# Kernel optimization log

Measured on AMD Instinct MI355X. Metric: run time of the kernel, lower is better.

Reference implementation:

```python
import jax, jax.numpy as jnp
import numpy as np

B, S, T = 16, 128, 128
V_SRC = V_TGT = 32000
E = H = 512
NL = 4


def setup_inputs() -> dict:
    key = jax.random.key(0)
    ks = jax.random.split(key, 16)
    sc = 0.05
    return {
        "src": jax.random.randint(ks[0], (B, S), 0, V_SRC),
        "tgt": jax.random.randint(ks[1], (B, T), 0, V_TGT),
        "src_emb": jax.random.normal(ks[2], (V_SRC, E), jnp.float32) * sc,
        "tgt_emb": jax.random.normal(ks[3], (V_TGT, E), jnp.float32) * sc,
        # stacked per-layer LSTM params (E == H so all layers share shape)
        "enc_Wih": jax.random.normal(ks[4], (NL, 4 * H, E), jnp.float32) * sc,
        "enc_Whh": jax.random.normal(ks[5], (NL, 4 * H, H), jnp.float32) * sc,
        "enc_b": jax.random.normal(ks[6], (NL, 4 * H), jnp.float32) * sc,
        "dec_Wih": jax.random.normal(ks[7], (NL, 4 * H, E), jnp.float32) * sc,
        "dec_Whh": jax.random.normal(ks[8], (NL, 4 * H, H), jnp.float32) * sc,
        "dec_b": jax.random.normal(ks[9], (NL, 4 * H), jnp.float32) * sc,
        "fc_W": jax.random.normal(ks[10], (V_TGT, H), jnp.float32) * sc,
        "fc_b": jax.random.normal(ks[11], (V_TGT,), jnp.float32) * sc,
    }


def _lstm_layer(x, Wih, Whh, b, h0, c0):
    # x: [B,T,E]; PyTorch gate order i,f,g,o. Input GEMM hoisted out of scan.
    xW = jnp.einsum("bte,ge->btg", x, Wih) + b  # [B,T,4H]

    def step(carry, xw):
        h, c = carry
        g = xw + h @ Whh.T
        i, f, gg, o = jnp.split(g, 4, axis=-1)
        c = jax.nn.sigmoid(f) * c + jax.nn.sigmoid(i) * jnp.tanh(gg)
        h = jax.nn.sigmoid(o) * jnp.tanh(c)
        return (h, c), h

    (hT, cT), hs = jax.lax.scan(step, (h0, c0), jnp.swapaxes(xW, 0, 1))
    return jnp.swapaxes(hs, 0, 1), hT, cT


def _lstm_stack(x, Wih, Whh, b, h0s, c0s):
    hTs, cTs = [], []
    for l in range(NL):
        x, hT, cT = _lstm_layer(x, Wih[l], Whh[l], b[l], h0s[l], c0s[l])
        hTs.append(hT)
        cTs.append(cT)
    return x, jnp.stack(hTs), jnp.stack(cTs)


def reference(src, tgt, src_emb, tgt_emb, enc_Wih, enc_Whh, enc_b,
              dec_Wih, dec_Whh, dec_b, fc_W, fc_b):
    zeros = jnp.zeros((NL, B, H), jnp.float32)
    # encoder
    _, hN, cN = _lstm_stack(src_emb[src], enc_Wih, enc_Whh, enc_b, zeros, zeros)
    # decoder initialized from encoder final state (train branch)
    dec_out, _, _ = _lstm_stack(tgt_emb[tgt], dec_Wih, dec_Whh, dec_b, hN, cN)
    # vocab projection
    return dec_out @ fc_W.T + fc_b  # [B,T,V_TGT]
```

## Files before the change

kernel.cpp:

```cpp
#include <hip/hip_runtime.h>
#include <hip/hip_bf16.h>
#include <cstddef>

#define NL   4
#define BB   16
#define TT   128
#define HH   512
#define G4   2048
#define BT   2048
#define VV   32000

__global__ __launch_bounds__(128) void embed_kern(const int* __restrict__ idx,
                                                  const float* __restrict__ emb,
                                                  float* __restrict__ out) {
  int tk = blockIdx.x;
  int row = idx[tk];
  const float4* s = (const float4*)(emb + (size_t)row * HH);
  float4* d = (float4*)(out + (size_t)tk * HH);
  d[threadIdx.x] = s[threadIdx.x];
}

__global__ __launch_bounds__(256) void zero_kern(float* __restrict__ p, int n) {
  int i = blockIdx.x * 256 + threadIdx.x;
  if (i < n) p[i] = 0.f;
}
__global__ __launch_bounds__(256) void copy_kern(float* __restrict__ d,
                                                 const float* __restrict__ s, int n) {
  int i = blockIdx.x * 256 + threadIdx.x;
  if (i < n) d[i] = s[i];
}

#define BM 128
#define BN 64
#define BK 16
__global__ __launch_bounds__(256) void gemm_bias_kern(
    const float* __restrict__ A, const float* __restrict__ B,
    const float* __restrict__ bias, float* __restrict__ C,
    int M, int N, int K)
{
  __shared__ float As[BK][BM];
  __shared__ float Bs[BK][BN];
  const int tid = threadIdx.x;
  const int m0 = blockIdx.y * BM;
  const int n0 = blockIdx.x * BN;
  const int ty = tid >> 4;
  const int tx = tid & 15;

  float acc[8][4];
#pragma unroll
  for (int i = 0; i < 8; ++i)
#pragma unroll
    for (int j = 0; j < 4; ++j) acc[i][j] = 0.f;

  for (int k0 = 0; k0 < K; k0 += BK) {
#pragma unroll
    for (int i = 0; i < 2; ++i) {
      int f = tid * 2 + i;
      int row = f >> 2;
      int k4 = (f & 3) * 4;
      float4 v = *(const float4*)(A + (size_t)(m0 + row) * K + k0 + k4);
      As[k4 + 0][row] = v.x;
      As[k4 + 1][row] = v.y;
      As[k4 + 2][row] = v.z;
      As[k4 + 3][row] = v.w;
    }
    {
      int row = tid >> 2;
      int k4 = (tid & 3) * 4;
      float4 v = *(const float4*)(B + (size_t)(n0 + row) * K + k0 + k4);
      Bs[k4 + 0][row] = v.x;
      Bs[k4 + 1][row] = v.y;
      Bs[k4 + 2][row] = v.z;
      Bs[k4 + 3][row] = v.w;
    }
    __syncthreads();
#pragma unroll
    for (int k = 0; k < BK; ++k) {
      float4 a0 = *(const float4*)&As[k][ty * 8];
      float4 a1 = *(const float4*)&As[k][ty * 8 + 4];
      float4 bv = *(const float4*)&Bs[k][tx * 4];
      float av[8] = {a0.x, a0.y, a0.z, a0.w, a1.x, a1.y, a1.z, a1.w};
      float bb[4] = {bv.x, bv.y, bv.z, bv.w};
#pragma unroll
      for (int i = 0; i < 8; ++i)
#pragma unroll
        for (int j = 0; j < 4; ++j) acc[i][j] += av[i] * bb[j];
    }
    __syncthreads();
  }
#pragma unroll
  for (int i = 0; i < 8; ++i) {
    size_t row = (size_t)(m0 + ty * 8 + i);
#pragma unroll
    for (int j = 0; j < 4; ++j) {
      int col = n0 + tx * 4 + j;
      C[row * (size_t)N + col] = acc[i][j] + (bias ? bias[col] : 0.f);
    }
  }
}

#define HPAD 516
__global__ __launch_bounds__(256) void lstm_step_kern(
    const float* __restrict__ xW,
    const float* __restrict__ Whh,
    const float* __restrict__ h_in,
    float* __restrict__ h_out,
    float* __restrict__ c,
    float* __restrict__ hs_out,
    int t)
{
  __shared__ float sh[BB * HPAD];
  __shared__ float gsm[BB][17];
  const int tid = threadIdx.x;
  const int j0 = blockIdx.x * 4;

#pragma unroll
  for (int i = 0; i < 8; ++i) {
    int f = tid + 256 * i;
    int row = f >> 7;
    int c4 = (f & 127) * 4;
    float4 v = *(const float4*)(h_in + (size_t)row * HH + c4);
    *(float4*)&sh[row * HPAD + c4] = v;
  }
  __syncthreads();

  const int b = tid >> 4;
  const int cl = tid & 15;
  const int g = cl >> 2;
  const int u = cl & 3;
  const int gcol = g * HH + j0 + u;

  const float* __restrict__ wrow = Whh + (size_t)gcol * HH;
  const float* __restrict__ hrow = sh + b * HPAD;

  float acc = xW[(size_t)(b * TT + t) * G4 + gcol];
  float acc2 = 0.f;
#pragma unroll 8
  for (int k = 0; k < HH; k += 8) {
    float4 w0 = *(const float4*)(wrow + k);
    float4 h0 = *(const float4*)(hrow + k);
    float4 w1 = *(const float4*)(wrow + k + 4);
    float4 h1 = *(const float4*)(hrow + k + 4);
    acc  += w0.x * h0.x + w0.y * h0.y + w0.z * h0.z + w0.w * h0.w;
    acc2 += w1.x * h1.x + w1.y * h1.y + w1.z * h1.z + w1.w * h1.w;
  }
  gsm[b][cl] = acc + acc2;
  __syncthreads();

  if (cl < 4) {
    int j = j0 + cl;
    float iv = gsm[b][cl];
    float fv = gsm[b][4 + cl];
    float gv = gsm[b][8 + cl];
    float ov = gsm[b][12 + cl];
    float cv = c[b * HH + j];
    float si = 1.f / (1.f + expf(-iv));
    float sf = 1.f / (1.f + expf(-fv));
    float so = 1.f / (1.f + expf(-ov));
    float tg = tanhf(gv);
    float cn = sf * cv + si * tg;
    float hn = so * tanhf(cn);
    c[b * HH + j] = cn;
    h_out[b * HH + j] = hn;
    hs_out[(size_t)(b * TT + t) * HH + j] = hn;
  }
}

extern "C" void kernel_launch(void* const* d_in, const int* in_sizes, int n_in,
                              void* d_out, int out_size, void* d_ws, size_t ws_size,
                              hipStream_t stream) {
  const int*   src     = (const int*)d_in[0];
  const int*   tgt     = (const int*)d_in[1];
  const float* src_emb = (const float*)d_in[2];
  const float* tgt_emb = (const float*)d_in[3];
  const float* enc_Wih = (const float*)d_in[4];
  const float* enc_Whh = (const float*)d_in[5];
  const float* enc_b   = (const float*)d_in[6];
  const float* dec_Wih = (const float*)d_in[7];
  const float* dec_Whh = (const float*)d_in[8];
  const float* dec_b   = (const float*)d_in[9];
  const float* fc_W    = (const float*)d_in[10];
  const float* fc_b    = (const float*)d_in[11];
  float* out = (float*)d_out;

  float* ws = (float*)d_ws;
  float* srcx  = ws;                 ws += (size_t)BT * HH;
  float* tgtx  = ws;                 ws += (size_t)BT * HH;
  float* hsA   = ws;                 ws += (size_t)BT * HH;
  float* hsB   = ws;                 ws += (size_t)BT * HH;
  float* xW    = ws;                 ws += (size_t)BT * G4;
  float* hping = ws;                 ws += BB * HH;
  float* hpong = ws;                 ws += BB * HH;
  float* cbuf  = ws;                 ws += BB * HH;
  float* finh  = ws;                 ws += NL * BB * HH;
  float* finc  = ws;                 ws += NL * BB * HH;

  embed_kern<<<BT, 128, 0, stream>>>(src, src_emb, srcx);
  embed_kern<<<BT, 128, 0, stream>>>(tgt, tgt_emb, tgtx);

  const int stateN = BB * HH;
  const int stateGrid = (stateN + 255) / 256;

  const float* dec_out = nullptr;

  for (int stack = 0; stack < 2; ++stack) {
    const float* Wih  = stack ? dec_Wih : enc_Wih;
    const float* Whh  = stack ? dec_Whh : enc_Whh;
    const float* bia  = stack ? dec_b   : enc_b;
    const float* curX = stack ? tgtx    : srcx;

    for (int l = 0; l < NL; ++l) {
      float* hs_out = (l & 1) ? hsB : hsA;

      {
        dim3 grid(G4 / BN, BT / BM);
        gemm_bias_kern<<<grid, 256, 0, stream>>>(
            curX, Wih + (size_t)l * G4 * HH, bia + (size_t)l * G4, xW,
            BT, G4, HH);
      }

      if (stack == 0) {
        zero_kern<<<stateGrid, 256, 0, stream>>>(hping, stateN);
        zero_kern<<<stateGrid, 256, 0, stream>>>(cbuf, stateN);
      } else {
        copy_kern<<<stateGrid, 256, 0, stream>>>(hping, finh + (size_t)l * stateN, stateN);
        copy_kern<<<stateGrid, 256, 0, stream>>>(cbuf,  finc + (size_t)l * stateN, stateN);
      }

      for (int t = 0; t < TT; ++t) {
        float* hin  = (t & 1) ? hpong : hping;
        float* hout = (t & 1) ? hping : hpong;
        lstm_step_kern<<<HH / 4, 256, 0, stream>>>(
            xW, Whh + (size_t)l * G4 * HH, hin, hout, cbuf, hs_out, t);
      }

      if (stack == 0) {
        copy_kern<<<stateGrid, 256, 0, stream>>>(finh + (size_t)l * stateN, hping, stateN);
        copy_kern<<<stateGrid, 256, 0, stream>>>(finc + (size_t)l * stateN, cbuf, stateN);
      }

      curX = hs_out;
      if (stack == 1 && l == NL - 1) dec_out = hs_out;
    }
  }

  {
    dim3 grid(VV / BN, BT / BM);
    gemm_bias_kern<<<grid, 256, 0, stream>>>(dec_out, fc_W, fc_b, out, BT, VV, HH);
  }
}
```

Before: 19.52 ms.

## Replace per-timestep LSTM launches with persistent kernel using grid barrier

Runs each LSTM layer's full recurrence inside one persistent kernel of 256 blocks, with a global atomic barrier between timesteps instead of one launch per step. Each block keeps its slice of Whh in registers across all steps and holds the cell state in shared memory, so weights and c are not reloaded every step. Gate partial sums are reduced with wave shuffles. The cost removed is per-step launch overhead and repeated weight reads. The risks are spin-barrier latency and relying on all 256 blocks being resident at once.

```diff
diff --git a/kernel.cpp b/kernel.cpp
--- a/kernel.cpp
+++ b/kernel.cpp
@@ -100,69 +100,140 @@
 }
 
 #define HPAD 516
-__global__ __launch_bounds__(256) void lstm_step_kern(
+__global__ __launch_bounds__(256) void lstm_layer_persist(
     const float* __restrict__ xW,
     const float* __restrict__ Whh,
-    const float* __restrict__ h_in,
-    float* __restrict__ h_out,
-    float* __restrict__ c,
+    const float* __restrict__ c_init,
+    float* __restrict__ h0,
+    float* __restrict__ h1,
     float* __restrict__ hs_out,
-    int t)
+    float* __restrict__ fin_h,
+    float* __restrict__ fin_c,
+    unsigned* __restrict__ bar,
+    unsigned step_base)
 {
+  const int tid  = threadIdx.x;
+  const int bid  = blockIdx.x;
+  const int wave = tid >> 6;
+  const int lane = tid & 63;
+  const int b4   = lane & 3;
+  const int ks   = lane >> 2;
+  const int j0   = bid * 2;
+  const int col0 = wave * HH + j0;
+
   __shared__ float sh[BB * HPAD];
-  __shared__ float gsm[BB][17];
-  const int tid = threadIdx.x;
-  const int j0 = blockIdx.x * 4;
-
-#pragma unroll
-  for (int i = 0; i < 8; ++i) {
-    int f = tid + 256 * i;
-    int row = f >> 7;
-    int c4 = (f & 127) * 4;
-    float4 v = *(const float4*)(h_in + (size_t)row * HH + c4);
-    *(float4*)&sh[row * HPAD + c4] = v;
+  __shared__ float gl[4][2][16];
+  __shared__ float cl[2][16];
+
+  float4 wv[2][8];
+#pragma unroll
+  for (int c = 0; c < 2; ++c)
+#pragma unroll
+    for (int j = 0; j < 8; ++j)
+      wv[c][j] = *(const float4*)(Whh + (size_t)(col0 + c) * HH + 4 * ks + 64 * j);
+
+  if (tid < 32) {
+    int u = tid >> 4, b = tid & 15;
+    cl[u][b] = c_init ? c_init[b * HH + j0 + u] : 0.f;
   }
   __syncthreads();
 
-  const int b = tid >> 4;
-  const int cl = tid & 15;
-  const int g = cl >> 2;
-  const int u = cl & 3;
-  const int gcol = g * HH + j0 + u;
-
-  const float* __restrict__ wrow = Whh + (size_t)gcol * HH;
-  const float* __restrict__ hrow = sh + b * HPAD;
-
-  float acc = xW[(size_t)(b * TT + t) * G4 + gcol];
-  float acc2 = 0.f;
-#pragma unroll 8
-  for (int k = 0; k < HH; k += 8) {
-    float4 w0 = *(const float4*)(wrow + k);
-    float4 h0 = *(const float4*)(hrow + k);
-    float4 w1 = *(const float4*)(wrow + k + 4);
-    float4 h1 = *(const float4*)(hrow + k + 4);
-    acc  += w0.x * h0.x + w0.y * h0.y + w0.z * h0.z + w0.w * h0.w;
-    acc2 += w1.x * h1.x + w1.y * h1.y + w1.z * h1.z + w1.w * h1.w;
-  }
-  gsm[b][cl] = acc + acc2;
-  __syncthreads();
-
-  if (cl < 4) {
-    int j = j0 + cl;
-    float iv = gsm[b][cl];
-    float fv = gsm[b][4 + cl];
-    float gv = gsm[b][8 + cl];
-    float ov = gsm[b][12 + cl];
-    float cv = c[b * HH + j];
-    float si = 1.f / (1.f + expf(-iv));
-    float sf = 1.f / (1.f + expf(-fv));
-    float so = 1.f / (1.f + expf(-ov));
-    float tg = tanhf(gv);
-    float cn = sf * cv + si * tg;
-    float hn = so * tanhf(cn);
-    c[b * HH + j] = cn;
-    h_out[b * HH + j] = hn;
-    hs_out[(size_t)(b * TT + t) * HH + j] = hn;
+  for (int t = 0; t < TT; ++t) {
+    const float* hin = (t & 1) ? h1 : h0;
+    float*       hout = (t & 1) ? h0 : h1;
+
+#pragma unroll
+    for (int i = 0; i < 8; ++i) {
+      int f = tid + 256 * i;
+      int row = f >> 7;
+      int c4 = (f & 127) << 2;
+      *(float4*)&sh[row * HPAD + c4] = *(const float4*)(hin + (size_t)row * HH + c4);
+    }
+
+    float acc[2][4];
+#pragma unroll
+    for (int c = 0; c < 2; ++c)
+#pragma unroll
+      for (int i = 0; i < 4; ++i) acc[c][i] = 0.f;
+    if (ks == 0) {
+#pragma unroll
+      for (int i = 0; i < 4; ++i) {
+        int b = b4 + 4 * i;
+        const float* xwp = xW + (size_t)(b * TT + t) * G4 + col0;
+        acc[0][i] = xwp[0];
+        acc[1][i] = xwp[1];
+      }
+    }
+    __syncthreads();
+
+#pragma unroll
+    for (int j = 0; j < 8; ++j) {
+      int kb = 4 * ks + 64 * j;
+      float4 h4[4];
+#pragma unroll
+      for (int i = 0; i < 4; ++i)
+        h4[i] = *(const float4*)&sh[(b4 + 4 * i) * HPAD + kb];
+#pragma unroll
+      for (int c = 0; c < 2; ++c)
+#pragma unroll
+        for (int i = 0; i < 4; ++i)
+          acc[c][i] += wv[c][j].x * h4[i].x + wv[c][j].y * h4[i].y +
+                       wv[c][j].z * h4[i].z + wv[c][j].w * h4[i].w;
+    }
+
+#pragma unroll
+    for (int off = 4; off < 64; off <<= 1) {
+#pragma unroll
+      for (int c = 0; c < 2; ++c)
+#pragma unroll
+        for (int i = 0; i < 4; ++i)
+          acc[c][i] += __shfl_xor(acc[c][i], off);
+    }
+
+    if (lane < 16) {
+      int i = lane >> 2;
+      gl[wave][0][lane] = acc[0][i];
+      gl[wave][1][lane] = acc[1][i];
+    }
+    __syncthreads();
+
+    if (tid < 32) {
+      int u = tid >> 4, b = tid & 15, j = j0 + u;
+      float iv = gl[0][u][b];
+      float fv = gl[1][u][b];
+      float gv = gl[2][u][b];
+      float ov = gl[3][u][b];
+      float cv = cl[u][b];
+      float si = 1.f / (1.f + expf(-iv));
+      float sf = 1.f / (1.f + expf(-fv));
+      float so = 1.f / (1.f + expf(-ov));
+      float tg = tanhf(gv);
+      float cn = sf * cv + si * tg;
+      float hn = so * tanhf(cn);
+      cl[u][b] = cn;
+      hout[b * HH + j] = hn;
+      hs_out[(size_t)(b * TT + t) * HH + j] = hn;
+      if (fin_h && t == TT - 1) {
+        fin_h[b * HH + j] = hn;
+        fin_c[b * HH + j] = cn;
+      }
+    }
+    __syncthreads();
+
+    if (wave == 0) {
+      if (lane == 0) {
+        __threadfence();
+        atomicAdd(&bar[(bid & 7) * 16], 1u);
+      }
+      unsigned target = 32u * (step_base + (unsigned)t + 1u);
+      if (lane < 8) {
+        while (__hip_atomic_load(&bar[lane * 16], __ATOMIC_RELAXED,
+                                 __HIP_MEMORY_SCOPE_AGENT) < target)
+          __builtin_amdgcn_s_sleep(1);
+      }
+      __threadfence();
+    }
+    __syncthreads();
   }
 }
 
@@ -184,16 +255,18 @@
   float* out = (float*)d_out;
 
   float* ws = (float*)d_ws;
+  unsigned* bar = (unsigned*)ws;     ws += 128;
   float* srcx  = ws;                 ws += (size_t)BT * HH;
   float* tgtx  = ws;                 ws += (size_t)BT * HH;
   float* hsA   = ws;                 ws += (size_t)BT * HH;
   float* hsB   = ws;                 ws += (size_t)BT * HH;
   float* xW    = ws;                 ws += (size_t)BT * G4;
-  float* hping = ws;                 ws += BB * HH;
-  float* hpong = ws;                 ws += BB * HH;
-  float* cbuf  = ws;                 ws += BB * HH;
+  float* hbuf0 = ws;                 ws += BB * HH;
+  float* hbuf1 = ws;                 ws += BB * HH;
   float* finh  = ws;                 ws += NL * BB * HH;
   float* finc  = ws;                 ws += NL * BB * HH;
+
+  zero_kern<<<1, 256, 0, stream>>>((float*)bar, 128);
 
   embed_kern<<<BT, 128, 0, stream>>>(src, src_emb, srcx);
   embed_kern<<<BT, 128, 0, stream>>>(tgt, tgt_emb, tgtx);
@@ -220,24 +293,19 @@
       }
 
       if (stack == 0) {
-        zero_kern<<<stateGrid, 256, 0, stream>>>(hping, stateN);
-        zero_kern<<<stateGrid, 256, 0, stream>>>(cbuf, stateN);
+        zero_kern<<<stateGrid, 256, 0, stream>>>(hbuf0, stateN);
       } else {
-        copy_kern<<<stateGrid, 256, 0, stream>>>(hping, finh + (size_t)l * stateN, stateN);
-        copy_kern<<<stateGrid, 256, 0, stream>>>(cbuf,  finc + (size_t)l * stateN, stateN);
-      }
-
-      for (int t = 0; t < TT; ++t) {
-        float* hin  = (t & 1) ? hpong : hping;
-        float* hout = (t & 1) ? hping : hpong;
-        lstm_step_kern<<<HH / 4, 256, 0, stream>>>(
-            xW, Whh + (size_t)l * G4 * HH, hin, hout, cbuf, hs_out, t);
-      }
-
-      if (stack == 0) {
-        copy_kern<<<stateGrid, 256, 0, stream>>>(finh + (size_t)l * stateN, hping, stateN);
-        copy_kern<<<stateGrid, 256, 0, stream>>>(finc + (size_t)l * stateN, cbuf, stateN);
-      }
+        copy_kern<<<stateGrid, 256, 0, stream>>>(hbuf0, finh + (size_t)l * stateN, stateN);
+      }
+
+      const float* cinit = stack ? (finc + (size_t)l * stateN) : nullptr;
+      float* fh = stack ? nullptr : (finh + (size_t)l * stateN);
+      float* fc = stack ? nullptr : (finc + (size_t)l * stateN);
+      unsigned step_base = (unsigned)((stack * NL + l) * TT);
+
+      lstm_layer_persist<<<256, 256, 0, stream>>>(
+          xW, Whh + (size_t)l * G4 * HH, cinit, hbuf0, hbuf1, hs_out,
+          fh, fc, bar, step_base);
 
       curX = hs_out;
       if (stack == 1 && l == NL - 1) dec_out = hs_out;
```

Result: slower. 21.52 ms (+10.2%).
